# Kernel optimization log

Measured on AMD Instinct MI355X. Metric: run time of the kernel, lower is better.

## Reference

```python
import jax, jax.numpy as jnp
import numpy as np

# Symmetric per-tensor int8 fake-quant (dynamic scale), the math that the
# q/k/v/smax matmul-act hooks and the matmul-error hooks apply in QAT mode.
# (With the module's default nn.Identity() hooks this reduces to identity;
# here we model the quantized path the module is designed for.)
QMAX = 127.0

def fake_quant(x):
    s = jnp.max(jnp.abs(x)) / QMAX + 1e-8
    return jnp.clip(jnp.round(x / s), -QMAX, QMAX) * s


def setup_inputs() -> dict:
    key = jax.random.key(0)
    ks = jax.random.split(key, 6)
    T, B, D = 2048, 2, 1024
    std = 0.02
    return {
        "x": jax.random.normal(ks[0], (T, B, D), dtype=jnp.float32),
        "wq": jax.random.normal(ks[1], (D, D), dtype=jnp.float32) * std,
        "bq": jnp.zeros((D,), dtype=jnp.float32),
        "wk": jax.random.normal(ks[2], (D, D), dtype=jnp.float32) * std,
        "bk": jnp.zeros((D,), dtype=jnp.float32),
        "wv": jax.random.normal(ks[3], (D, D), dtype=jnp.float32) * std,
        "bv": jnp.zeros((D,), dtype=jnp.float32),
        "wo": jax.random.normal(ks[4], (D, D), dtype=jnp.float32) * std,
        "bo": jnp.zeros((D,), dtype=jnp.float32),
        "num_heads": 16,
    }


def reference(x, wq, bq, wk, bk, wv, bv, wo, bo, num_heads):
    # x: (T, B, D)  -- fairseq Time x Batch x Channel layout
    T, B, D = x.shape
    H = num_heads
    Dh = D // H
    scaling = Dh ** -0.5

    q = (x @ wq.T + bq) * scaling          # (T, B, D)
    k = x @ wk.T + bk
    v = x @ wv.T + bv

    # view(T, B*H, Dh).transpose(0,1) -> (B*H, T, Dh)
    q = q.reshape(T, B * H, Dh).transpose(1, 0, 2)
    k = k.reshape(T, B * H, Dh).transpose(1, 0, 2)
    v = v.reshape(T, B * H, Dh).transpose(1, 0, 2)

    # attn_weights = k_q_err_quant( bmm(q_act_quant(q), k_act_quant(k)^T) )
    scores = fake_quant(jnp.einsum('bqd,bkd->bqk', fake_quant(q), fake_quant(k)))
    probs = jax.nn.softmax(scores, axis=-1)  # dropout p=0.0

    # attn = smax_v_err_quant( bmm(smax_act_quant(probs), v_act_quant(v)) )
    attn = fake_quant(jnp.einsum('bqk,bkd->bqd', fake_quant(probs), fake_quant(v)))

    attn = attn.transpose(1, 0, 2).reshape(T, B, D)  # back to (T, B, D)
    out = attn @ wo.T + bo
    return out
```

## Files before the change

### kernel.cpp

```cpp
#include <hip/hip_runtime.h>
#include <stdint.h>

#define T_DIM 2048
#define B_DIM 2
#define D_DIM 1024
#define H_DIM 16
#define DH    64
#define G_DIM 32
#define N_ROWS 4096
#define K_DIM 1024

typedef __bf16 bf16x8 __attribute__((ext_vector_type(8)));
typedef float  f32x4  __attribute__((ext_vector_type(4)));
typedef int    i32x4  __attribute__((ext_vector_type(4)));

typedef const __attribute__((address_space(1))) unsigned int* gas_u32;
typedef __attribute__((address_space(3))) unsigned int* las_u32;

static __device__ __forceinline__ void gload16(const void* gsrc, void* ldst) {
  __builtin_amdgcn_global_load_lds((gas_u32)gsrc, (las_u32)ldst, 16, 0, 0);
}

static __device__ __forceinline__ unsigned short f32_to_bf16_rne(float f) {
  unsigned u = __float_as_uint(f);
  u += 0x7FFFu + ((u >> 16) & 1u);
  return (unsigned short)(u >> 16);
}
static __device__ __forceinline__ float bf16_to_f32(unsigned short h) {
  return __uint_as_float(((unsigned)h) << 16);
}

static __device__ __forceinline__ void split4_store(const float* __restrict__ src,
                                                    unsigned short* __restrict__ hi,
                                                    unsigned short* __restrict__ lo,
                                                    size_t i4) {
  float4 x = *reinterpret_cast<const float4*>(src + i4);
  ushort4 h, l;
  { float f = x.x; h.x = f32_to_bf16_rne(f); l.x = f32_to_bf16_rne(f - bf16_to_f32(h.x)); }
  { float f = x.y; h.y = f32_to_bf16_rne(f); l.y = f32_to_bf16_rne(f - bf16_to_f32(h.y)); }
  { float f = x.z; h.z = f32_to_bf16_rne(f); l.z = f32_to_bf16_rne(f - bf16_to_f32(h.z)); }
  { float f = x.w; h.w = f32_to_bf16_rne(f); l.w = f32_to_bf16_rne(f - bf16_to_f32(h.w)); }
  *reinterpret_cast<ushort4*>(hi + i4) = h;
  *reinterpret_cast<ushort4*>(lo + i4) = l;
}

__global__ __launch_bounds__(256) void split_x_kernel(const float* __restrict__ src,
                                                      unsigned short* __restrict__ hi,
                                                      unsigned short* __restrict__ lo) {
  size_t i4 = ((size_t)blockIdx.x * 256 + threadIdx.x) * 4;
  split4_store(src, hi, lo, i4);
}

__global__ __launch_bounds__(256) void split_w_kernel(const float* __restrict__ w0,
                                                      const float* __restrict__ w1,
                                                      const float* __restrict__ w2,
                                                      const float* __restrict__ w3,
                                                      unsigned short* __restrict__ hi,
                                                      unsigned short* __restrict__ lo) {
  const int z = blockIdx.z;
  const float* src = (z == 0) ? w0 : (z == 1) ? w1 : (z == 2) ? w2 : w3;
  size_t base = (size_t)z * (D_DIM * D_DIM);
  size_t i4 = ((size_t)blockIdx.x * 256 + threadIdx.x) * 4;
  split4_store(src, hi + base, lo + base, i4);
}

__global__ __launch_bounds__(256) void gemm_bf16x3_v2(
    const unsigned short* __restrict__ Ahi, const unsigned short* __restrict__ Alo,
    const unsigned short* __restrict__ Whi, const unsigned short* __restrict__ Wlo,
    const float* __restrict__ b0, const float* __restrict__ b1, const float* __restrict__ b2,
    float* __restrict__ C, int ncols, unsigned* __restrict__ scal_base, float alpha0) {
  __shared__ __align__(16) unsigned short sAh[128 * 64];
  __shared__ __align__(16) unsigned short sAl[128 * 64];
  __shared__ __align__(16) unsigned short sWh[64 * 64];
  __shared__ __align__(16) unsigned short sWl[64 * 64];
  __shared__ unsigned sam;
  const int lane = threadIdx.x & 63, wave = threadIdx.x >> 6;
  const int ntn = ncols >> 6;
  const int cpx = gridDim.x >> 3;
  const int bid = blockIdx.x;
  const int swz = (bid & 7) * cpx + (bid >> 3);
  const int tm = swz / ntn, tn = swz - tm * ntn;
  const int rowBase = tm * 128, colBase = tn * 64;
  const int wr = wave >> 1, wc = wave & 1;
  const int lr = lane >> 3, lk = (lane & 7) * 8;
  const int lo = lane & 15, hi4 = lane >> 4;

  f32x4 acc[4][2];
#pragma unroll
  for (int i = 0; i < 4; ++i)
#pragma unroll
    for (int j = 0; j < 2; ++j) acc[i][j] = f32x4{0.f, 0.f, 0.f, 0.f};

  for (int k0 = 0; k0 < K_DIM; k0 += 64) {
    __syncthreads();
#pragma unroll
    for (int i = 0; i < 4; ++i) {
      const int ca = wave * 4 + i;
      const size_t go = (size_t)(rowBase + ca * 8 + lr) * K_DIM + k0 + lk;
      gload16(Ahi + go, &sAh[ca * 512]);
      gload16(Alo + go, &sAl[ca * 512]);
    }
#pragma unroll
    for (int i = 0; i < 2; ++i) {
      const int cw = wave * 2 + i;
      const size_t go = (size_t)(colBase + cw * 8 + lr) * K_DIM + k0 + lk;
      gload16(Whi + go, &sWh[cw * 512]);
      gload16(Wlo + go, &sWl[cw * 512]);
    }
    __syncthreads();
#pragma unroll
    for (int kk = 0; kk < 64; kk += 32) {
      bf16x8 ah[4], al[4], wh[2], wl[2];
#pragma unroll
      for (int rt = 0; rt < 4; ++rt) {
        const int off = (wr * 64 + rt * 16 + lo) * 64 + kk + hi4 * 8;
        ah[rt] = *reinterpret_cast<const bf16x8*>(&sAh[off]);
        al[rt] = *reinterpret_cast<const bf16x8*>(&sAl[off]);
      }
#pragma unroll
      for (int jt = 0; jt < 2; ++jt) {
        const int off = (wc * 32 + jt * 16 + lo) * 64 + kk + hi4 * 8;
        wh[jt] = *reinterpret_cast<const bf16x8*>(&sWh[off]);
        wl[jt] = *reinterpret_cast<const bf16x8*>(&sWl[off]);
      }
#pragma unroll
      for (int jt = 0; jt < 2; ++jt)
#pragma unroll
        for (int rt = 0; rt < 4; ++rt) {
          acc[rt][jt] = __builtin_amdgcn_mfma_f32_16x16x32_bf16(ah[rt], wh[jt], acc[rt][jt], 0, 0, 0);
          acc[rt][jt] = __builtin_amdgcn_mfma_f32_16x16x32_bf16(ah[rt], wl[jt], acc[rt][jt], 0, 0, 0);
          acc[rt][jt] = __builtin_amdgcn_mfma_f32_16x16x32_bf16(al[rt], wh[jt], acc[rt][jt], 0, 0, 0);
        }
    }
  }
  const int sec = colBase >> 10;
  const float* bp = (sec == 0) ? b0 : ((sec == 1) ? b1 : b2);
  const float alpha = (sec == 0) ? alpha0 : 1.0f;
  const int colL = (colBase & 1023) + wc * 32;
  float bj[2];
#pragma unroll
  for (int jt = 0; jt < 2; ++jt) bj[jt] = bp[colL + jt * 16 + lo];
  float am = 0.f;
#pragma unroll
  for (int rt = 0; rt < 4; ++rt)
#pragma unroll
    for (int jt = 0; jt < 2; ++jt)
#pragma unroll
      for (int r = 0; r < 4; ++r) {
        float v = (acc[rt][jt][r] + bj[jt]) * alpha;
        C[(size_t)(rowBase + wr * 64 + rt * 16 + hi4 * 4 + r) * ncols + colBase + wc * 32 +
          jt * 16 + lo] = v;
        am = fmaxf(am, fabsf(v));
      }
#pragma unroll
  for (int s = 32; s; s >>= 1) am = fmaxf(am, __shfl_xor(am, s));
  if (threadIdx.x == 0) sam = 0u;
  __syncthreads();
  if (lane == 0) atomicMax(&sam, __float_as_uint(am));
  __syncthreads();
  if (threadIdx.x == 0) atomicMax(scal_base + sec, sam);
}

__global__ __launch_bounds__(256) void quant_qk_kernel(const float* __restrict__ qkv32,
                                                       signed char* __restrict__ qi8,
                                                       signed char* __restrict__ ki8,
                                                       unsigned* __restrict__ scal) {
  if (blockIdx.x == 0 && blockIdx.y == 0 && threadIdx.x == 0) scal[4] = 0x7F800000u;
  const int which = blockIdx.y;
  signed char* dst = which ? ki8 : qi8;
  const float s = __uint_as_float(scal[which]) / 127.0f + 1e-8f;
  size_t i4 = ((size_t)blockIdx.x * 256 + threadIdx.x) * 4;
  int d = (int)(i4 & (D_DIM - 1));
  int row = (int)(i4 >> 10);
  float4 x = *reinterpret_cast<const float4*>(qkv32 + (size_t)row * 3072 + which * 1024 + d);
  int t = row >> 1, b = row & 1;
  int h = d >> 6, dh = d & 63;
  char4 c;
  { float q = rintf(x.x / s); q = fminf(127.f, fmaxf(-127.f, q)); c.x = (signed char)q; }
  { float q = rintf(x.y / s); q = fminf(127.f, fmaxf(-127.f, q)); c.y = (signed char)q; }
  { float q = rintf(x.z / s); q = fminf(127.f, fmaxf(-127.f, q)); c.z = (signed char)q; }
  { float q = rintf(x.w / s); q = fminf(127.f, fmaxf(-127.f, q)); c.w = (signed char)q; }
  *reinterpret_cast<char4*>(dst + (((size_t)(b * H_DIM + h) * T_DIM + t) * DH + dh)) = c;
}

__global__ __launch_bounds__(256) void quant_v_kernel(const float* __restrict__ qkv32,
                                                      signed char* __restrict__ viT8,
                                                      const unsigned* __restrict__ scal) {
  const float s = __uint_as_float(scal[2]) / 127.0f + 1e-8f;
  const int g = blockIdx.y, t0 = blockIdx.x * 64;
  const int b = g >> 4, h = g & 15;
  __shared__ signed char tile[64][68];
  const int tid = threadIdx.x;
#pragma unroll
  for (int rep = 0; rep < 4; ++rep) {
    int tl = tid >> 2;
    int f4 = (tid & 3) + rep * 4;
    const float* p = qkv32 + ((size_t)(t0 + tl) * B_DIM + b) * 3072 + 2048 + h * 64 + f4 * 4;
    float4 x = *reinterpret_cast<const float4*>(p);
    char4 c;
    { float q = rintf(x.x / s); q = fminf(127.f, fmaxf(-127.f, q)); c.x = (signed char)q; }
    { float q = rintf(x.y / s); q = fminf(127.f, fmaxf(-127.f, q)); c.y = (signed char)q; }
    { float q = rintf(x.z / s); q = fminf(127.f, fmaxf(-127.f, q)); c.z = (signed char)q; }
    { float q = rintf(x.w / s); q = fminf(127.f, fmaxf(-127.f, q)); c.w = (signed char)q; }
    *reinterpret_cast<char4*>(&tile[tl][f4 * 4]) = c;
  }
  __syncthreads();
  const int dh = tid >> 2, tq = tid & 3;
  signed char outb[16];
#pragma unroll
  for (int j = 0; j < 16; ++j) outb[j] = tile[tq * 16 + j][dh];
  i32x4 vv;
  __builtin_memcpy(&vv, outb, 16);
  *reinterpret_cast<i32x4*>(viT8 + ((size_t)g * DH + dh) * T_DIM + t0 + tq * 16) = vv;
}

static __device__ __forceinline__ void xpose4(int h, int& p0, int& p1, int& p2, int& p3) {
  const bool b0 = (h & 1), b1 = (h & 2);
  int s0 = __shfl_xor(p0, 16), s1 = __shfl_xor(p1, 16);
  int s2 = __shfl_xor(p2, 16), s3 = __shfl_xor(p3, 16);
  int q0 = b0 ? s1 : p0;
  int q1 = b0 ? p1 : s0;
  int q2 = b0 ? s3 : p2;
  int q3 = b0 ? p3 : s2;
  int u0 = __shfl_xor(q0, 32), u1 = __shfl_xor(q1, 32);
  int u2 = __shfl_xor(q2, 32), u3 = __shfl_xor(q3, 32);
  p0 = b1 ? u2 : q0;
  p1 = b1 ? u3 : q1;
  p2 = b1 ? q2 : u0;
  p3 = b1 ? q3 : u1;
}

__global__ __launch_bounds__(256) void attn_smax_kernel(const signed char* __restrict__ qi8,
                                                        const signed char* __restrict__ ki8,
                                                        unsigned* __restrict__ scal) {
  const int lane = threadIdx.x & 63, wave = threadIdx.x >> 6;
  const int g = blockIdx.y;
  const int qb = blockIdx.x * 64 + wave * 16;
  const int lo = lane & 15, hi4 = lane >> 4;
  const signed char* qg = qi8 + (size_t)g * T_DIM * DH;
  const signed char* kg = ki8 + (size_t)g * T_DIM * DH;
  const i32x4 qfr = *reinterpret_cast<const i32x4*>(qg + (size_t)(qb + lo) * DH + hi4 * 16);
  const i32x4 zero = {0, 0, 0, 0};
  int mx = -2147483647, mn = 2147483647;
#pragma unroll 4
  for (int kc = 0; kc < T_DIM; kc += 16) {
    i32x4 kfr = *reinterpret_cast<const i32x4*>(kg + (size_t)(kc + lo) * DH + hi4 * 16);
    i32x4 sc = __builtin_amdgcn_mfma_i32_16x16x64_i8(kfr, qfr, zero, 0, 0, 0);
#pragma unroll
    for (int r = 0; r < 4; ++r) { mx = sc[r] > mx ? sc[r] : mx; mn = sc[r] < mn ? sc[r] : mn; }
  }
  int am = mx > -mn ? mx : -mn;
#pragma unroll
  for (int s = 32; s; s >>= 1) { int o = __shfl_xor(am, s); am = o > am ? o : am; }
  __shared__ int sm;
  if (threadIdx.x == 0) sm = 0;
  __syncthreads();
  if (lane == 0) atomicMax(&sm, am);
  __syncthreads();
  if (threadIdx.x == 0) atomicMax((int*)&scal[3], sm);
}

__global__ __launch_bounds__(256) void attn_stats_kernel(const signed char* __restrict__ qi8,
                                                         const signed char* __restrict__ ki8,
                                                         unsigned* __restrict__ scal,
                                                         float* __restrict__ rowZ,
                                                         float* __restrict__ rowL) {
  const float sq = __uint_as_float(scal[0]) / 127.0f + 1e-8f;
  const float sk = __uint_as_float(scal[1]) / 127.0f + 1e-8f;
  const float sqsk = sq * sk;
  const float smax = sqsk * (float)(int)scal[3];
  const float s_s = smax / 127.0f + 1e-8f;
  const float ratio = sqsk / s_s;
  const float a = s_s * 1.4426950408889634f;
  const float c = -127.0f * a;
  const int lane = threadIdx.x & 63, wave = threadIdx.x >> 6;
  const int g = blockIdx.y;
  const int qb = blockIdx.x * 64 + wave * 16;
  const int lo = lane & 15, hi4 = lane >> 4;
  const signed char* qg = qi8 + (size_t)g * T_DIM * DH;
  const signed char* kg = ki8 + (size_t)g * T_DIM * DH;
  const i32x4 qfr = *reinterpret_cast<const i32x4*>(qg + (size_t)(qb + lo) * DH + hi4 * 16);
  const i32x4 zero = {0, 0, 0, 0};
  float mx = -1e30f, zp = 0.f;
#pragma unroll 4
  for (int kc = 0; kc < T_DIM; kc += 16) {
    i32x4 kfr = *reinterpret_cast<const i32x4*>(kg + (size_t)(kc + lo) * DH + hi4 * 16);
    i32x4 sc = __builtin_amdgcn_mfma_i32_16x16x64_i8(kfr, qfr, zero, 0, 0, 0);
#pragma unroll
    for (int r = 0; r < 4; ++r) {
      float lf = rintf((float)sc[r] * ratio);
      mx = fmaxf(mx, lf);
      zp += exp2f(fmaf(lf, a, c));
    }
  }
  mx = fmaxf(mx, __shfl_xor(mx, 16)); zp += __shfl_xor(zp, 16);
  mx = fmaxf(mx, __shfl_xor(mx, 32)); zp += __shfl_xor(zp, 32);
  float Z = zp * exp2f((127.0f - mx) * a);
  if (hi4 == 0) {
    rowZ[(size_t)g * T_DIM + qb + lo] = Z;
    rowL[(size_t)g * T_DIM + qb + lo] = mx;
  }
  float zm = Z;
#pragma unroll
  for (int s = 32; s; s >>= 1) zm = fminf(zm, __shfl_xor(zm, s));
  __shared__ unsigned szm;
  if (threadIdx.x == 0) szm = 0x7F800000u;
  __syncthreads();
  if (lane == 0) atomicMin(&szm, __float_as_uint(zm));
  __syncthreads();
  if (threadIdx.x == 0) atomicMin(&scal[4], szm);
}

__global__ __launch_bounds__(256) void attn_pv_kernel(const signed char* __restrict__ qi8,
                                                      const signed char* __restrict__ ki8,
                                                      const signed char* __restrict__ viT8,
                                                      const float* __restrict__ rowZ,
                                                      const float* __restrict__ rowL,
                                                      unsigned* __restrict__ scal,
                                                      int* __restrict__ attn_out) {
  const float sq = __uint_as_float(scal[0]) / 127.0f + 1e-8f;
  const float sk = __uint_as_float(scal[1]) / 127.0f + 1e-8f;
  const float sqsk = sq * sk;
  const float smax = sqsk * (float)(int)scal[3];
  const float s_s = smax / 127.0f + 1e-8f;
  const float ratio = sqsk / s_s;
  const float a = s_s * 1.4426950408889634f;
  const float maxp = 1.0f / __uint_as_float(scal[4]);
  const float s_p = maxp / 127.0f + 1e-8f;
  const float inv_sp = 1.0f / s_p;
  const int lane = threadIdx.x & 63, wave = threadIdx.x >> 6;
  const int g = blockIdx.y;
  const int qb = blockIdx.x * 64 + wave * 16;
  const int lo = lane & 15, hi4 = lane >> 4;
  const signed char* qg = qi8 + (size_t)g * T_DIM * DH;
  const signed char* kg = ki8 + (size_t)g * T_DIM * DH;
  const signed char* vg = viT8 + (size_t)g * DH * T_DIM;
  const i32x4 qfr = *reinterpret_cast<const i32x4*>(qg + (size_t)(qb + lo) * DH + hi4 * 16);
  const float rz = 1.0f / rowZ[(size_t)g * T_DIM + qb + lo];
  const float crow = rz * inv_sp;
  const float bneg = -rowL[(size_t)g * T_DIM + qb + lo] * a;
  const i32x4 zero = {0, 0, 0, 0};
  i32x4 accv[4];
#pragma unroll
  for (int dt = 0; dt < 4; ++dt) accv[dt] = zero;

  for (int kc = 0; kc < T_DIM; kc += 64) {
    int pk[4];
#pragma unroll
    for (int t = 0; t < 4; ++t) {
      i32x4 kfr =
          *reinterpret_cast<const i32x4*>(kg + (size_t)(kc + t * 16 + lo) * DH + hi4 * 16);
      i32x4 sc = __builtin_amdgcn_mfma_i32_16x16x64_i8(kfr, qfr, zero, 0, 0, 0);
      int ip[4];
#pragma unroll
      for (int r = 0; r < 4; ++r) {
        float lf = rintf((float)sc[r] * ratio);
        float e = exp2f(fmaf(lf, a, bneg));
        float pf = fminf(rintf(e * crow), 127.f);
        ip[r] = (int)pf;
      }
      pk[t] = (ip[0] & 255) | ((ip[1] & 255) << 8) | ((ip[2] & 255) << 16) | (ip[3] << 24);
    }
    xpose4(hi4, pk[0], pk[1], pk[2], pk[3]);
    const i32x4 pfr = {pk[0], pk[1], pk[2], pk[3]};
#pragma unroll
    for (int dt = 0; dt < 4; ++dt) {
      i32x4 vfr =
          *reinterpret_cast<const i32x4*>(vg + (size_t)(dt * 16 + lo) * T_DIM + kc + hi4 * 16);
      accv[dt] = __builtin_amdgcn_mfma_i32_16x16x64_i8(pfr, vfr, accv[dt], 0, 0, 0);
    }
  }
  int am = 0;
#pragma unroll
  for (int dt = 0; dt < 4; ++dt)
#pragma unroll
    for (int r = 0; r < 4; ++r) {
      int v = accv[dt][r];
      attn_out[((size_t)g * T_DIM + qb + hi4 * 4 + r) * DH + dt * 16 + lo] = v;
      int av = v < 0 ? -v : v;
      am = av > am ? av : am;
    }
#pragma unroll
  for (int s = 32; s; s >>= 1) { int o = __shfl_xor(am, s); am = o > am ? o : am; }
  __shared__ int sm;
  if (threadIdx.x == 0) sm = 0;
  __syncthreads();
  if (lane == 0) atomicMax(&sm, am);
  __syncthreads();
  if (threadIdx.x == 0) atomicMax((int*)&scal[5], sm);
}

__global__ __launch_bounds__(256) void quant_attn_kernel(const int* __restrict__ attn_i32,
                                                         unsigned short* __restrict__ aq_hi,
                                                         unsigned short* __restrict__ aq_lo,
                                                         const unsigned* __restrict__ scal) {
  const float sv = __uint_as_float(scal[2]) / 127.0f + 1e-8f;
  const float maxp = 1.0f / __uint_as_float(scal[4]);
  const float s_p = maxp / 127.0f + 1e-8f;
  const float spsv = s_p * sv;
  const float amax = spsv * (float)(int)scal[5];
  const float s_a = amax / 127.0f + 1e-8f;
  size_t i4 = ((size_t)blockIdx.x * 256 + threadIdx.x) * 4;
  i32x4 iv = *reinterpret_cast<const i32x4*>(attn_i32 + i4);
  int dh0 = (int)(i4 & 63);
  int t = (int)((i4 >> 6) & (T_DIM - 1));
  int g = (int)(i4 >> 17);
  int b = g >> 4, h = g & 15;
  ushort4 hh, ll;
  { float v = (float)iv[0] * spsv; float lf = fminf(127.f, fmaxf(-127.f, rintf(v / s_a)));
    float qv = lf * s_a; hh.x = f32_to_bf16_rne(qv); ll.x = f32_to_bf16_rne(qv - bf16_to_f32(hh.x)); }
  { float v = (float)iv[1] * spsv; float lf = fminf(127.f, fmaxf(-127.f, rintf(v / s_a)));
    float qv = lf * s_a; hh.y = f32_to_bf16_rne(qv); ll.y = f32_to_bf16_rne(qv - bf16_to_f32(hh.y)); }
  { float v = (float)iv[2] * spsv; float lf = fminf(127.f, fmaxf(-127.f, rintf(v / s_a)));
    float qv = lf * s_a; hh.z = f32_to_bf16_rne(qv); ll.z = f32_to_bf16_rne(qv - bf16_to_f32(hh.z)); }
  { float v = (float)iv[3] * spsv; float lf = fminf(127.f, fmaxf(-127.f, rintf(v / s_a)));
    float qv = lf * s_a; hh.w = f32_to_bf16_rne(qv); ll.w = f32_to_bf16_rne(qv - bf16_to_f32(hh.w)); }
  size_t o = (size_t)(t * B_DIM + b) * D_DIM + h * 64 + dh0;
  *reinterpret_cast<ushort4*>(aq_hi + o) = hh;
  *reinterpret_cast<ushort4*>(aq_lo + o) = ll;
}

extern "C" void kernel_launch(void* const* d_in, const int* in_sizes, int n_in,
                              void* d_out, int out_size, void* d_ws, size_t ws_size,
                              hipStream_t stream) {
  (void)in_sizes; (void)n_in; (void)out_size;
  const float* x  = (const float*)d_in[0];
  const float* wq = (const float*)d_in[1];
  const float* bq = (const float*)d_in[2];
  const float* wk = (const float*)d_in[3];
  const float* bk = (const float*)d_in[4];
  const float* wv = (const float*)d_in[5];
  const float* bv = (const float*)d_in[6];
  const float* wo = (const float*)d_in[7];
  const float* bo = (const float*)d_in[8];
  float* out = (float*)d_out;
  char* ws = (char*)d_ws;

  constexpr size_t SZ_ROW   = (size_t)G_DIM * T_DIM * 4;
  constexpr size_t SZ_XSPL  = (size_t)N_ROWS * D_DIM * 2;
  constexpr size_t SZ_WSPL  = (size_t)4 * D_DIM * D_DIM * 2;
  constexpr size_t SZ_QKV   = (size_t)N_ROWS * 3072 * 4;
  constexpr size_t SZ_I8    = (size_t)G_DIM * T_DIM * DH;
  constexpr size_t OFF_ROWZ = 256;
  constexpr size_t OFF_ROWL = OFF_ROWZ + SZ_ROW;
  constexpr size_t OFF_XHI  = OFF_ROWL + SZ_ROW;
  constexpr size_t OFF_XLO  = OFF_XHI + SZ_XSPL;
  constexpr size_t OFF_WHI  = OFF_XLO + SZ_XSPL;
  constexpr size_t OFF_WLO  = OFF_WHI + SZ_WSPL;
  constexpr size_t OFF_QKV  = OFF_WLO + SZ_WSPL;
  constexpr size_t OFF_QI8  = OFF_QKV + SZ_QKV;
  constexpr size_t OFF_KI8  = OFF_QI8 + SZ_I8;
  constexpr size_t OFF_VIT8 = OFF_KI8 + SZ_I8;
  constexpr size_t OFF_END  = OFF_VIT8 + SZ_I8;
  if (ws_size < OFF_END) return;

  unsigned* scal = (unsigned*)ws;
  float* rowZ = (float*)(ws + OFF_ROWZ);
  float* rowL = (float*)(ws + OFF_ROWL);
  unsigned short* x_hi = (unsigned short*)(ws + OFF_XHI);
  unsigned short* x_lo = (unsigned short*)(ws + OFF_XLO);
  unsigned short* w_hi = (unsigned short*)(ws + OFF_WHI);
  unsigned short* w_lo = (unsigned short*)(ws + OFF_WLO);
  float* qkv32 = (float*)(ws + OFF_QKV);
  signed char* qi8 = (signed char*)(ws + OFF_QI8);
  signed char* ki8 = (signed char*)(ws + OFF_KI8);
  signed char* viT8 = (signed char*)(ws + OFF_VIT8);
  int* attn_i32 = (int*)(ws + OFF_QKV);
  unsigned short* aq_hi = x_hi;
  unsigned short* aq_lo = x_lo;

  hipMemsetAsync(ws, 0, 64, stream);
  split_x_kernel<<<4096, 256, 0, stream>>>(x, x_hi, x_lo);
  split_w_kernel<<<dim3(1024, 1, 4), 256, 0, stream>>>(wq, wk, wv, wo, w_hi, w_lo);
  gemm_bf16x3_v2<<<1536, 256, 0, stream>>>(x_hi, x_lo, w_hi, w_lo, bq, bk, bv, qkv32, 3072,
                                           scal, 0.125f);
  quant_qk_kernel<<<dim3(4096, 2), 256, 0, stream>>>(qkv32, qi8, ki8, scal);
  quant_v_kernel<<<dim3(32, 32), 256, 0, stream>>>(qkv32, viT8, scal);
  attn_smax_kernel<<<dim3(32, 32), 256, 0, stream>>>(qi8, ki8, scal);
  attn_stats_kernel<<<dim3(32, 32), 256, 0, stream>>>(qi8, ki8, scal, rowZ, rowL);
  attn_pv_kernel<<<dim3(32, 32), 256, 0, stream>>>(qi8, ki8, viT8, rowZ, rowL, scal, attn_i32);
  quant_attn_kernel<<<4096, 256, 0, stream>>>(attn_i32, aq_hi, aq_lo, scal);
  gemm_bf16x3_v2<<<512, 256, 0, stream>>>(aq_hi, aq_lo, w_hi + 3145728, w_lo + 3145728, bo, bo,
                                          bo, out, 1024, scal + 6, 1.0f);
}
```

Before: 438.1 us.

## Widen GEMM tiles to 128x128 and replace softmax exp with LDS lookup tables

The bf16x3 GEMM tile grows from 128x64 to 128x128 per block, which halves the grid and raises operand reuse per LDS load. The MFMA issue order is regrouped into three passes. The attention stats and PV kernels swap per-element exp2 evaluation for shared-memory lookup tables indexed by the quantized score (a per-block table in stats, a per-row table in PV), and stats tracks the integer max instead of the float max. This trades transcendental work for LDS gathers, plus per-block table setup and higher register and LDS use in the GEMM.

```diff
diff --git a/kernel.cpp b/kernel.cpp
--- a/kernel.cpp
+++ b/kernel.cpp
@@ -64,32 +64,32 @@
   split4_store(src, hi + base, lo + base, i4);
 }
 
-__global__ __launch_bounds__(256) void gemm_bf16x3_v2(
+__global__ __launch_bounds__(256, 2) void gemm_bf16x3_v3(
     const unsigned short* __restrict__ Ahi, const unsigned short* __restrict__ Alo,
     const unsigned short* __restrict__ Whi, const unsigned short* __restrict__ Wlo,
     const float* __restrict__ b0, const float* __restrict__ b1, const float* __restrict__ b2,
     float* __restrict__ C, int ncols, unsigned* __restrict__ scal_base, float alpha0) {
   __shared__ __align__(16) unsigned short sAh[128 * 64];
   __shared__ __align__(16) unsigned short sAl[128 * 64];
-  __shared__ __align__(16) unsigned short sWh[64 * 64];
-  __shared__ __align__(16) unsigned short sWl[64 * 64];
+  __shared__ __align__(16) unsigned short sWh[128 * 64];
+  __shared__ __align__(16) unsigned short sWl[128 * 64];
   __shared__ unsigned sam;
   const int lane = threadIdx.x & 63, wave = threadIdx.x >> 6;
-  const int ntn = ncols >> 6;
+  const int ntn = ncols >> 7;
   const int cpx = gridDim.x >> 3;
   const int bid = blockIdx.x;
   const int swz = (bid & 7) * cpx + (bid >> 3);
   const int tm = swz / ntn, tn = swz - tm * ntn;
-  const int rowBase = tm * 128, colBase = tn * 64;
+  const int rowBase = tm * 128, colBase = tn * 128;
   const int wr = wave >> 1, wc = wave & 1;
   const int lr = lane >> 3, lk = (lane & 7) * 8;
   const int lo = lane & 15, hi4 = lane >> 4;
 
-  f32x4 acc[4][2];
+  f32x4 acc[4][4];
 #pragma unroll
   for (int i = 0; i < 4; ++i)
 #pragma unroll
-    for (int j = 0; j < 2; ++j) acc[i][j] = f32x4{0.f, 0.f, 0.f, 0.f};
+    for (int j = 0; j < 4; ++j) acc[i][j] = f32x4{0.f, 0.f, 0.f, 0.f};
 
   for (int k0 = 0; k0 < K_DIM; k0 += 64) {
     __syncthreads();
@@ -99,56 +99,56 @@
       const size_t go = (size_t)(rowBase + ca * 8 + lr) * K_DIM + k0 + lk;
       gload16(Ahi + go, &sAh[ca * 512]);
       gload16(Alo + go, &sAl[ca * 512]);
-    }
-#pragma unroll
-    for (int i = 0; i < 2; ++i) {
-      const int cw = wave * 2 + i;
-      const size_t go = (size_t)(colBase + cw * 8 + lr) * K_DIM + k0 + lk;
-      gload16(Whi + go, &sWh[cw * 512]);
-      gload16(Wlo + go, &sWl[cw * 512]);
+      const size_t gw = (size_t)(colBase + ca * 8 + lr) * K_DIM + k0 + lk;
+      gload16(Whi + gw, &sWh[ca * 512]);
+      gload16(Wlo + gw, &sWl[ca * 512]);
     }
     __syncthreads();
 #pragma unroll
     for (int kk = 0; kk < 64; kk += 32) {
-      bf16x8 ah[4], al[4], wh[2], wl[2];
+      bf16x8 ah[4], al[4], wh[4], wl[4];
 #pragma unroll
       for (int rt = 0; rt < 4; ++rt) {
-        const int off = (wr * 64 + rt * 16 + lo) * 64 + kk + hi4 * 8;
-        ah[rt] = *reinterpret_cast<const bf16x8*>(&sAh[off]);
-        al[rt] = *reinterpret_cast<const bf16x8*>(&sAl[off]);
+        const int offA = (wr * 64 + rt * 16 + lo) * 64 + kk + hi4 * 8;
+        ah[rt] = *reinterpret_cast<const bf16x8*>(&sAh[offA]);
+        al[rt] = *reinterpret_cast<const bf16x8*>(&sAl[offA]);
+        const int offW = (wc * 64 + rt * 16 + lo) * 64 + kk + hi4 * 8;
+        wh[rt] = *reinterpret_cast<const bf16x8*>(&sWh[offW]);
+        wl[rt] = *reinterpret_cast<const bf16x8*>(&sWl[offW]);
       }
 #pragma unroll
-      for (int jt = 0; jt < 2; ++jt) {
-        const int off = (wc * 32 + jt * 16 + lo) * 64 + kk + hi4 * 8;
-        wh[jt] = *reinterpret_cast<const bf16x8*>(&sWh[off]);
-        wl[jt] = *reinterpret_cast<const bf16x8*>(&sWl[off]);
-      }
-#pragma unroll
-      for (int jt = 0; jt < 2; ++jt)
-#pragma unroll
-        for (int rt = 0; rt < 4; ++rt) {
+      for (int jt = 0; jt < 4; ++jt)
+#pragma unroll
+        for (int rt = 0; rt < 4; ++rt)
           acc[rt][jt] = __builtin_amdgcn_mfma_f32_16x16x32_bf16(ah[rt], wh[jt], acc[rt][jt], 0, 0, 0);
+#pragma unroll
+      for (int jt = 0; jt < 4; ++jt)
+#pragma unroll
+        for (int rt = 0; rt < 4; ++rt)
           acc[rt][jt] = __builtin_amdgcn_mfma_f32_16x16x32_bf16(ah[rt], wl[jt], acc[rt][jt], 0, 0, 0);
+#pragma unroll
+      for (int jt = 0; jt < 4; ++jt)
+#pragma unroll
+        for (int rt = 0; rt < 4; ++rt)
           acc[rt][jt] = __builtin_amdgcn_mfma_f32_16x16x32_bf16(al[rt], wh[jt], acc[rt][jt], 0, 0, 0);
-        }
     }
   }
   const int sec = colBase >> 10;
   const float* bp = (sec == 0) ? b0 : ((sec == 1) ? b1 : b2);
   const float alpha = (sec == 0) ? alpha0 : 1.0f;
-  const int colL = (colBase & 1023) + wc * 32;
-  float bj[2];
-#pragma unroll
-  for (int jt = 0; jt < 2; ++jt) bj[jt] = bp[colL + jt * 16 + lo];
+  const int colL = (colBase & 1023) + wc * 64;
+  float bj[4];
+#pragma unroll
+  for (int jt = 0; jt < 4; ++jt) bj[jt] = bp[colL + jt * 16 + lo];
   float am = 0.f;
 #pragma unroll
   for (int rt = 0; rt < 4; ++rt)
 #pragma unroll
-    for (int jt = 0; jt < 2; ++jt)
+    for (int jt = 0; jt < 4; ++jt)
 #pragma unroll
       for (int r = 0; r < 4; ++r) {
         float v = (acc[rt][jt][r] + bj[jt]) * alpha;
-        C[(size_t)(rowBase + wr * 64 + rt * 16 + hi4 * 4 + r) * ncols + colBase + wc * 32 +
+        C[(size_t)(rowBase + wr * 64 + rt * 16 + hi4 * 4 + r) * ncols + colBase + wc * 64 +
           jt * 16 + lo] = v;
         am = fmaxf(am, fabsf(v));
       }
@@ -273,7 +273,11 @@
   const float ratio = sqsk / s_s;
   const float a = s_s * 1.4426950408889634f;
   const float c = -127.0f * a;
-  const int lane = threadIdx.x & 63, wave = threadIdx.x >> 6;
+  __shared__ float gLut[256];
+  const int tid = threadIdx.x;
+  if (tid < 255) gLut[tid] = exp2f(fmaf((float)(tid - 127), a, c));
+  __syncthreads();
+  const int lane = tid & 63, wave = tid >> 6;
   const int g = blockIdx.y;
   const int qb = blockIdx.x * 64 + wave * 16;
   const int lo = lane & 15, hi4 = lane >> 4;
@@ -281,20 +285,24 @@
   const signed char* kg = ki8 + (size_t)g * T_DIM * DH;
   const i32x4 qfr = *reinterpret_cast<const i32x4*>(qg + (size_t)(qb + lo) * DH + hi4 * 16);
   const i32x4 zero = {0, 0, 0, 0};
-  float mx = -1e30f, zp = 0.f;
+  int scmax = -2147483647;
+  float zp = 0.f;
 #pragma unroll 4
   for (int kc = 0; kc < T_DIM; kc += 16) {
     i32x4 kfr = *reinterpret_cast<const i32x4*>(kg + (size_t)(kc + lo) * DH + hi4 * 16);
     i32x4 sc = __builtin_amdgcn_mfma_i32_16x16x64_i8(kfr, qfr, zero, 0, 0, 0);
 #pragma unroll
     for (int r = 0; r < 4; ++r) {
-      float lf = rintf((float)sc[r] * ratio);
-      mx = fmaxf(mx, lf);
-      zp += exp2f(fmaf(lf, a, c));
-    }
-  }
-  mx = fmaxf(mx, __shfl_xor(mx, 16)); zp += __shfl_xor(zp, 16);
-  mx = fmaxf(mx, __shfl_xor(mx, 32)); zp += __shfl_xor(zp, 32);
+      scmax = sc[r] > scmax ? sc[r] : scmax;
+      int idx = (int)rintf((float)sc[r] * ratio) + 127;
+      zp += gLut[idx];
+    }
+  }
+  { int o = __shfl_xor(scmax, 16); scmax = o > scmax ? o : scmax; }
+  zp += __shfl_xor(zp, 16);
+  { int o = __shfl_xor(scmax, 32); scmax = o > scmax ? o : scmax; }
+  zp += __shfl_xor(zp, 32);
+  float mx = rintf((float)scmax * ratio);
   float Z = zp * exp2f((127.0f - mx) * a);
   if (hi4 == 0) {
     rowZ[(size_t)g * T_DIM + qb + lo] = Z;
@@ -304,13 +312,14 @@
 #pragma unroll
   for (int s = 32; s; s >>= 1) zm = fminf(zm, __shfl_xor(zm, s));
   __shared__ unsigned szm;
-  if (threadIdx.x == 0) szm = 0x7F800000u;
+  if (tid == 0) szm = 0x7F800000u;
   __syncthreads();
   if (lane == 0) atomicMin(&szm, __float_as_uint(zm));
   __syncthreads();
-  if (threadIdx.x == 0) atomicMin(&scal[4], szm);
-}
-
+  if (tid == 0) atomicMin(&scal[4], szm);
+}
+
+#define LUTS 260
 __global__ __launch_bounds__(256) void attn_pv_kernel(const signed char* __restrict__ qi8,
                                                       const signed char* __restrict__ ki8,
                                                       const signed char* __restrict__ viT8,
@@ -328,17 +337,34 @@
   const float maxp = 1.0f / __uint_as_float(scal[4]);
   const float s_p = maxp / 127.0f + 1e-8f;
   const float inv_sp = 1.0f / s_p;
-  const int lane = threadIdx.x & 63, wave = threadIdx.x >> 6;
+  const int tid = threadIdx.x;
+  const int lane = tid & 63, wave = tid >> 6;
   const int g = blockIdx.y;
-  const int qb = blockIdx.x * 64 + wave * 16;
+  const int qb0 = blockIdx.x * 64;
+  const int qb = qb0 + wave * 16;
   const int lo = lane & 15, hi4 = lane >> 4;
+
+  __shared__ signed char plut[64 * LUTS];
+  for (int n = tid; n < 64 * 256; n += 256) {
+    const int row = n >> 8, i = n & 255;
+    if (i < 255) {
+      const float Zr = rowZ[(size_t)g * T_DIM + qb0 + row];
+      const float lm = rowL[(size_t)g * T_DIM + qb0 + row];
+      const float crow = (1.0f / Zr) * inv_sp;
+      const float bneg = -lm * a;
+      const float lf = (float)(i - 127);
+      const float e = exp2f(fmaf(lf, a, bneg));
+      const float pf = fminf(rintf(e * crow), 127.f);
+      plut[row * LUTS + i] = (signed char)(int)pf;
+    }
+  }
+  __syncthreads();
+
   const signed char* qg = qi8 + (size_t)g * T_DIM * DH;
   const signed char* kg = ki8 + (size_t)g * T_DIM * DH;
   const signed char* vg = viT8 + (size_t)g * DH * T_DIM;
   const i32x4 qfr = *reinterpret_cast<const i32x4*>(qg + (size_t)(qb + lo) * DH + hi4 * 16);
-  const float rz = 1.0f / rowZ[(size_t)g * T_DIM + qb + lo];
-  const float crow = rz * inv_sp;
-  const float bneg = -rowL[(size_t)g * T_DIM + qb + lo] * a;
+  const int lbase = (wave * 16 + lo) * LUTS + 127;
   const i32x4 zero = {0, 0, 0, 0};
   i32x4 accv[4];
 #pragma unroll
@@ -351,15 +377,12 @@
       i32x4 kfr =
           *reinterpret_cast<const i32x4*>(kg + (size_t)(kc + t * 16 + lo) * DH + hi4 * 16);
       i32x4 sc = __builtin_amdgcn_mfma_i32_16x16x64_i8(kfr, qfr, zero, 0, 0, 0);
-      int ip[4];
-#pragma unroll
-      for (int r = 0; r < 4; ++r) {
-        float lf = rintf((float)sc[r] * ratio);
-        float e = exp2f(fmaf(lf, a, bneg));
-        float pf = fminf(rintf(e * crow), 127.f);
-        ip[r] = (int)pf;
-      }
-      pk[t] = (ip[0] & 255) | ((ip[1] & 255) << 8) | ((ip[2] & 255) << 16) | (ip[3] << 24);
+      unsigned b0, b1, b2, b3;
+      { int idx = (int)rintf((float)sc[0] * ratio); b0 = (unsigned char)plut[lbase + idx]; }
+      { int idx = (int)rintf((float)sc[1] * ratio); b1 = (unsigned char)plut[lbase + idx]; }
+      { int idx = (int)rintf((float)sc[2] * ratio); b2 = (unsigned char)plut[lbase + idx]; }
+      { int idx = (int)rintf((float)sc[3] * ratio); b3 = (unsigned char)plut[lbase + idx]; }
+      pk[t] = (int)(b0 | (b1 << 8) | (b2 << 16) | (b3 << 24));
     }
     xpose4(hi4, pk[0], pk[1], pk[2], pk[3]);
     const i32x4 pfr = {pk[0], pk[1], pk[2], pk[3]};
@@ -383,11 +406,11 @@
 #pragma unroll
   for (int s = 32; s; s >>= 1) { int o = __shfl_xor(am, s); am = o > am ? o : am; }
   __shared__ int sm;
-  if (threadIdx.x == 0) sm = 0;
+  if (tid == 0) sm = 0;
   __syncthreads();
   if (lane == 0) atomicMax(&sm, am);
   __syncthreads();
-  if (threadIdx.x == 0) atomicMax((int*)&scal[5], sm);
+  if (tid == 0) atomicMax((int*)&scal[5], sm);
 }
 
 __global__ __launch_bounds__(256) void quant_attn_kernel(const int* __restrict__ attn_i32,
@@ -472,14 +495,14 @@
   hipMemsetAsync(ws, 0, 64, stream);
   split_x_kernel<<<4096, 256, 0, stream>>>(x, x_hi, x_lo);
   split_w_kernel<<<dim3(1024, 1, 4), 256, 0, stream>>>(wq, wk, wv, wo, w_hi, w_lo);
-  gemm_bf16x3_v2<<<1536, 256, 0, stream>>>(x_hi, x_lo, w_hi, w_lo, bq, bk, bv, qkv32, 3072,
-                                           scal, 0.125f);
+  gemm_bf16x3_v3<<<768, 256, 0, stream>>>(x_hi, x_lo, w_hi, w_lo, bq, bk, bv, qkv32, 3072,
+                                          scal, 0.125f);
   quant_qk_kernel<<<dim3(4096, 2), 256, 0, stream>>>(qkv32, qi8, ki8, scal);
   quant_v_kernel<<<dim3(32, 32), 256, 0, stream>>>(qkv32, viT8, scal);
   attn_smax_kernel<<<dim3(32, 32), 256, 0, stream>>>(qi8, ki8, scal);
   attn_stats_kernel<<<dim3(32, 32), 256, 0, stream>>>(qi8, ki8, scal, rowZ, rowL);
   attn_pv_kernel<<<dim3(32, 32), 256, 0, stream>>>(qi8, ki8, viT8, rowZ, rowL, scal, attn_i32);
   quant_attn_kernel<<<4096, 256, 0, stream>>>(attn_i32, aq_hi, aq_lo, scal);
-  gemm_bf16x3_v2<<<512, 256, 0, stream>>>(aq_hi, aq_lo, w_hi + 3145728, w_lo + 3145728, bo, bo,
+  gemm_bf16x3_v3<<<256, 256, 0, stream>>>(aq_hi, aq_lo, w_hi + 3145728, w_lo + 3145728, bo, bo,
                                           bo, out, 1024, scal + 6, 1.0f);
 }
```

Measured after the change: 429.7 us. Within noise of the previous version (-1.9%).
